# Kernel tuning notes

Hardware: AMD Instinct MI355X
Metric: run time of the kernel (lower is better)

## Reference

```python
import jax, jax.numpy as jnp
import numpy as np
import math

N_EDGES = 3
N_HEADS = 2
ITERS = 2
NEG = -1e9


def setup_inputs() -> dict:
    key = jax.random.key(0)
    ks = jax.random.split(key, 8)
    B, N, D = 4, 2048, 256
    E, H, I = N_EDGES, N_HEADS, ITERS
    s = 1.0 / math.sqrt(D)
    return {
        "nodes_embed": jax.random.normal(ks[0], (B, N, D), jnp.float32),
        "node_adj": jax.random.randint(ks[1], (B, N, N), 0, E + 1, jnp.int32),
        "Wq": jax.random.normal(ks[2], (E, D, D), jnp.float32) * s,
        "bq": jnp.zeros((E, D), jnp.float32),
        "Wk": jax.random.normal(ks[3], (E, D, D), jnp.float32) * s,
        "bk": jnp.zeros((E, D), jnp.float32),
        "gcn_W": jax.random.normal(ks[4], (I, D, D), jnp.float32) * s,
        "gcn_b": jnp.zeros((I, D), jnp.float32),
        "agg_W": jax.random.normal(ks[5], (H * D, D), jnp.float32) * (1.0 / math.sqrt(H * D)),
        "agg_b": jnp.zeros((D,), jnp.float32),
    }


def _forward(nodes_embed, node_adj, Wq, bq, Wk, bk, gcn_W, gcn_b, agg_W, agg_b):
    B, N, D = nodes_embed.shape
    H = N_HEADS
    dk = D // H
    adj = node_adj[:, None]  # [B,1,N,N] broadcast over heads

    # Per-edge-type masked attention accumulation (scores init at 0).
    scores = jnp.zeros((B, H, N, N), nodes_embed.dtype)
    for e in range(N_EDGES):  # small fixed edge-type loop
        q = (nodes_embed @ Wq[e] + bq[e]).reshape(B, N, H, dk).transpose(0, 2, 1, 3)
        k = (nodes_embed @ Wk[e] + bk[e]).reshape(B, N, H, dk).transpose(0, 2, 1, 3)
        raw = jnp.einsum('bhnd,bhmd->bhnm', q, k) / math.sqrt(dk)
        scores = jnp.where(adj == e + 1, scores + raw, scores)

    # Positions never touched (adj==0 or no matching type) stay exactly 0 -> masked.
    scores = jnp.where(scores == 0.0, NEG, scores)
    attn = jax.nn.softmax(scores, axis=-1)  # [B,H,N,N]

    # Per-head GCN stack (parameters shared across heads, as in the torch code).
    outs = []
    for head in range(H):
        a = attn[:, head]  # [B,N,N]
        degs = jnp.sum(a, axis=-1, keepdims=True)  # [B,N,1]
        x = nodes_embed
        for i in range(ITERS):
            h1 = jnp.einsum('bnd,df->bnf', x, gcn_W[i])
            sum_nei = jnp.einsum('bnm,bmf->bnf', a, h1)
            x = x + jax.nn.relu(sum_nei / degs + gcn_b[i])
        outs.append(x)

    out = jnp.concatenate(outs, axis=-1) @ agg_W + agg_b  # [B,N,D]
    graph_attention = jnp.transpose(attn, (1, 0, 2, 3))  # [H,B,N,N]
    return out, graph_attention


def reference(nodes_embed, node_adj, Wq, bq, Wk, bk, gcn_W, gcn_b, agg_W, agg_b):
    return _forward(nodes_embed, node_adj, Wq, bq, Wk, bk, gcn_W, gcn_b, agg_W, agg_b)
```

## Files before the change

### kernel.cpp

```cpp
#include <hip/hip_runtime.h>
#include <stdint.h>
#include <stddef.h>


typedef unsigned short bf16_t;
typedef __attribute__((ext_vector_type(4))) float floatx4;
typedef __attribute__((ext_vector_type(8))) __bf16 bf16x8;
typedef __attribute__((ext_vector_type(4))) unsigned short u16x4;

#define NEGV -1000000000.0f

__device__ __forceinline__ bf16_t f2b(float f) {
  union { float f; uint32_t u; } v; v.f = f;
  uint32_t r = v.u + 0x7FFFu + ((v.u >> 16) & 1u);
  return (bf16_t)(r >> 16);
}

typedef __attribute__((address_space(1))) void gvoid_t;
typedef __attribute__((address_space(3))) void svoid_t;
__device__ __forceinline__ void gll16(const void* g, void* l) {
  __builtin_amdgcn_global_load_lds((gvoid_t*)(g), (svoid_t*)(l), 16, 0, 0);
}

__device__ __forceinline__ bf16x8 lds_frag(const bf16_t* base, int row, int quad) {
  return *(const bf16x8*)(base + (row << 5) + (((quad + (row >> 1)) & 3) << 3));
}

__device__ __forceinline__ void gemm_core(
    const bf16_t* __restrict__ A, int lda, int rowA0,
    const bf16_t* __restrict__ Bt, int ldb, int rowB0,
    int K, bf16_t* lA, bf16_t* lB, floatx4 acc[4][4])
{
  const int lane = threadIdx.x & 63;
  const int wave = threadIdx.x >> 6;
  const int l16  = lane & 15;
  const int quad = lane >> 4;
  const int wm = (wave >> 1) << 6;
  const int wn = (wave & 1) << 6;
  const int srow = (wave << 5) + (lane >> 2);
  const int scol = (((lane & 3) - (srow >> 1)) & 3) << 3;
  const bf16_t* gA0 = A + (size_t)(rowA0 + srow) * lda + scol;
  const bf16_t* gA1 = gA0 + (size_t)16 * lda;
  const bf16_t* gB0 = Bt + (size_t)(rowB0 + srow) * ldb + scol;
  const bf16_t* gB1 = gB0 + (size_t)16 * ldb;
  bf16_t* lA0 = lA + (wave << 5) * 32;
  bf16_t* lA1 = lA0 + 16 * 32;
  bf16_t* lB0 = lB + (wave << 5) * 32;
  bf16_t* lB1 = lB0 + 16 * 32;

  for (int k0 = 0; k0 < K; k0 += 32) {
    __syncthreads();
    gll16(gA0 + k0, lA0);
    gll16(gA1 + k0, lA1);
    gll16(gB0 + k0, lB0);
    gll16(gB1 + k0, lB1);
    __syncthreads();
    bf16x8 af[4], bv[4];
#pragma unroll
    for (int mi = 0; mi < 4; ++mi) af[mi] = lds_frag(lA, wm + mi * 16 + l16, quad);
#pragma unroll
    for (int ni = 0; ni < 4; ++ni) bv[ni] = lds_frag(lB, wn + ni * 16 + l16, quad);
#pragma unroll
    for (int mi = 0; mi < 4; ++mi)
#pragma unroll
      for (int ni = 0; ni < 4; ++ni)
        acc[mi][ni] = __builtin_amdgcn_mfma_f32_16x16x32_bf16(af[mi], bv[ni], acc[mi][ni], 0, 0, 0);
  }
}

__device__ __forceinline__ void gemm_core64(
    const bf16_t* __restrict__ A, int lda, int rowA0,
    const bf16_t* __restrict__ Bt, int ldb, int rowB0,
    int K, bf16_t* lA, bf16_t* lB, floatx4 acc[4][2])
{
  const int lane = threadIdx.x & 63;
  const int wave = threadIdx.x >> 6;
  const int l16  = lane & 15;
  const int quad = lane >> 4;
  const int wn   = wave << 5;
  const int tr   = (wave << 4) + (lane >> 2);
  const int scol = (((lane & 3) - (tr >> 1)) & 3) << 3;
  const bf16_t* gA  = A  + (size_t)(rowA0 + tr) * lda + scol;
  const bf16_t* gB0 = Bt + (size_t)(rowB0 + tr) * ldb + scol;
  const bf16_t* gB1 = gB0 + (size_t)64 * ldb;
  bf16_t* lAd = lA + (wave << 9);
  bf16_t* lB0 = lB + (wave << 9);
  bf16_t* lB1 = lB + 2048 + (wave << 9);

  for (int k0 = 0; k0 < K; k0 += 32) {
    __syncthreads();
    gll16(gA  + k0, lAd);
    gll16(gB0 + k0, lB0);
    gll16(gB1 + k0, lB1);
    __syncthreads();
    bf16x8 af[4], bv[2];
#pragma unroll
    for (int mi = 0; mi < 4; ++mi) af[mi] = lds_frag(lA, mi * 16 + l16, quad);
#pragma unroll
    for (int ni = 0; ni < 2; ++ni) bv[ni] = lds_frag(lB, wn + ni * 16 + l16, quad);
#pragma unroll
    for (int mi = 0; mi < 4; ++mi)
#pragma unroll
      for (int ni = 0; ni < 2; ++ni)
        acc[mi][ni] = __builtin_amdgcn_mfma_f32_16x16x32_bf16(af[mi], bv[ni], acc[mi][ni], 0, 0, 0);
  }
}

#define TILE_IDS \
  const int lane = threadIdx.x & 63; \
  const int wave = threadIdx.x >> 6; \
  const int l16  = lane & 15; \
  const int quad = lane >> 4; \
  const int wm = (wave >> 1) << 6; \
  const int wn = (wave & 1) << 6;

#define TILE_IDS64 \
  const int lane = threadIdx.x & 63; \
  const int wave = threadIdx.x >> 6; \
  const int l16  = lane & 15; \
  const int quad = lane >> 4; \
  const int wn = wave << 5;

#define ZERO44(acc) \
  { const floatx4 z4_ = {0.f, 0.f, 0.f, 0.f}; \
    for (int mi_ = 0; mi_ < 4; ++mi_) for (int ni_ = 0; ni_ < 4; ++ni_) acc[mi_][ni_] = z4_; }
#define ZERO42(acc) \
  { const floatx4 z4_ = {0.f, 0.f, 0.f, 0.f}; \
    for (int mi_ = 0; mi_ < 4; ++mi_) for (int ni_ = 0; ni_ < 2; ++ni_) acc[mi_][ni_] = z4_; }

__global__ __launch_bounds__(256) void k_cast_x(const float* __restrict__ x,
                                                bf16_t* __restrict__ xb) {
  int i = blockIdx.x * 256 + threadIdx.x;
  float4 a = ((const float4*)x)[i * 2];
  float4 b = ((const float4*)x)[i * 2 + 1];
  bf16_t o[8] = { f2b(a.x), f2b(a.y), f2b(a.z), f2b(a.w),
                  f2b(b.x), f2b(b.y), f2b(b.z), f2b(b.w) };
  ((uint4*)xb)[i] = *(uint4*)o;
}

__global__ __launch_bounds__(256) void k_cast_w(
    const float* __restrict__ Wq, const float* __restrict__ Wk,
    const float* __restrict__ gW, const float* __restrict__ aW,
    bf16_t* __restrict__ WqkT, bf16_t* __restrict__ gWT, bf16_t* __restrict__ aWT) {
  int idx = blockIdx.x * 256 + threadIdx.x;
  if (idx < 393216) {
    int zz = idx >> 16, r = idx & 65535;
    int n = r >> 8, k = r & 255;
    const float* src = (zz < 3) ? (Wq + (size_t)zz * 65536) : (Wk + (size_t)(zz - 3) * 65536);
    WqkT[idx] = f2b(src[k * 256 + n]);
  } else if (idx < 524288) {
    int t = idx - 393216;
    int i = t >> 16, r = t & 65535;
    int f = r >> 8, k = r & 255;
    gWT[t] = f2b(gW[(size_t)i * 65536 + k * 256 + f]);
  } else if (idx < 655360) {
    int t = idx - 524288;
    int f = t >> 9, k = t & 511;
    aWT[t] = f2b(aW[k * 256 + f]);
  }
}

__global__ __launch_bounds__(256) void k_gemm_proj(
    const bf16_t* __restrict__ xb, const bf16_t* __restrict__ WqkT,
    const float* __restrict__ bq, const float* __restrict__ bk,
    bf16_t* __restrict__ qcat, bf16_t* __restrict__ kcat) {
  __shared__ bf16_t lA[4096], lB[4096];
  int z = blockIdx.z;
  int e = (z < 3) ? z : z - 3;
  const bf16_t* Wz = WqkT + (size_t)z * 65536;
  const float* bias = ((z < 3) ? bq : bk) + e * 256;
  bf16_t* dst = (z < 3) ? qcat : kcat;
  int bm0 = blockIdx.y * 128, bn0 = blockIdx.x * 128;
  floatx4 acc[4][4];
  ZERO44(acc);
  gemm_core(xb, 256, bm0, Wz, 256, bn0, 256, lA, lB, acc);
  TILE_IDS;
#pragma unroll
  for (int mi = 0; mi < 4; ++mi)
#pragma unroll
    for (int ni = 0; ni < 4; ++ni)
#pragma unroll
      for (int r = 0; r < 4; ++r) {
        int row = bm0 + wm + mi * 16 + quad * 4 + r;
        int col = bn0 + wn + ni * 16 + l16;
        int b = row >> 11, n = row & 2047;
        int h = col >> 7, kk = col & 127;
        float v = acc[mi][ni][r] + bias[col];
        dst[((size_t)((b * 2 + h) * 2048 + n)) * 384 + e * 128 + kk] = f2b(v);
      }
}

__global__ __launch_bounds__(256) void k_scores(
    const bf16_t* __restrict__ qcat, const bf16_t* __restrict__ kcat,
    const int* __restrict__ adj, float* __restrict__ sc) {
  __shared__ bf16_t lA[2048], lB[4096];
  int z = blockIdx.z;
  int h = z >> 2, b = z & 3;
  const bf16_t* A  = qcat + (size_t)(b * 2 + h) * 2048 * 384;
  const bf16_t* Bt = kcat + (size_t)(b * 2 + h) * 2048 * 384;
  const int* adjb = adj + (size_t)b * 2048 * 2048;
  int bm0 = blockIdx.y * 64, bn0 = blockIdx.x * 128;
  TILE_IDS64;

  uint32_t adjv[4][2];
#pragma unroll
  for (int mi = 0; mi < 4; ++mi)
#pragma unroll
    for (int ni = 0; ni < 2; ++ni) {
      int col = bn0 + wn + ni * 16 + l16;
      uint32_t v = 0;
#pragma unroll
      for (int r = 0; r < 4; ++r) {
        int row = bm0 + mi * 16 + quad * 4 + r;
        v |= ((uint32_t)adjb[(size_t)row * 2048 + col] & 3u) << (r * 8);
      }
      adjv[mi][ni] = v;
    }

  floatx4 sel[4][2];
  ZERO42(sel);
  for (int e = 0; e < 3; ++e) {
    floatx4 acc[4][2];
    ZERO42(acc);
    gemm_core64(A + e * 128, 384, bm0, Bt + e * 128, 384, bn0, 128, lA, lB, acc);
#pragma unroll
    for (int mi = 0; mi < 4; ++mi)
#pragma unroll
      for (int ni = 0; ni < 2; ++ni) {
        uint32_t av = adjv[mi][ni];
#pragma unroll
        for (int r = 0; r < 4; ++r) {
          bool m = (((av >> (r * 8)) & 255u) == (uint32_t)(e + 1));
          sel[mi][ni][r] = m ? acc[mi][ni][r] : sel[mi][ni][r];
        }
      }
  }
  const float scale = 0.08838834764831845f;
#pragma unroll
  for (int mi = 0; mi < 4; ++mi)
#pragma unroll
    for (int ni = 0; ni < 2; ++ni)
#pragma unroll
      for (int r = 0; r < 4; ++r) {
        int row = bm0 + mi * 16 + quad * 4 + r;
        int col = bn0 + wn + ni * 16 + l16;
        uint32_t a = (adjv[mi][ni] >> (r * 8)) & 255u;
        float v = (a == 0u) ? NEGV : sel[mi][ni][r] * scale;
        sc[((size_t)z * 2048 + row) * 2048 + col] = v;
      }
}

__global__ __launch_bounds__(256) void k_softmax(float* __restrict__ sc,
                                                 bf16_t* __restrict__ abf) {
  int row = blockIdx.x * 4 + (threadIdx.x >> 6);
  int lane = threadIdx.x & 63;
  float4* p4 = (float4*)(sc + (size_t)row * 2048);
  float4 v[8];
  float mx = -3.4e38f;
#pragma unroll
  for (int j = 0; j < 8; ++j) {
    v[j] = p4[j * 64 + lane];
    mx = fmaxf(mx, fmaxf(fmaxf(v[j].x, v[j].y), fmaxf(v[j].z, v[j].w)));
  }
#pragma unroll
  for (int off = 32; off; off >>= 1) mx = fmaxf(mx, __shfl_xor(mx, off));
  float s = 0.f;
#pragma unroll
  for (int j = 0; j < 8; ++j) {
    v[j].x = __expf(v[j].x - mx); v[j].y = __expf(v[j].y - mx);
    v[j].z = __expf(v[j].z - mx); v[j].w = __expf(v[j].w - mx);
    s += v[j].x + v[j].y + v[j].z + v[j].w;
  }
#pragma unroll
  for (int off = 32; off; off >>= 1) s += __shfl_xor(s, off);
  float inv = 1.0f / s;
  u16x4* b4 = (u16x4*)(abf + (size_t)row * 2048);
#pragma unroll
  for (int j = 0; j < 8; ++j) {
    float4 o;
    o.x = v[j].x * inv; o.y = v[j].y * inv; o.z = v[j].z * inv; o.w = v[j].w * inv;
    p4[j * 64 + lane] = o;
    u16x4 ov = { f2b(o.x), f2b(o.y), f2b(o.z), f2b(o.w) };
    b4[j * 64 + lane] = ov;
  }
}

__global__ __launch_bounds__(256) void k_gemm_bf16T(
    const bf16_t* __restrict__ A, const bf16_t* __restrict__ Wt,
    bf16_t* __restrict__ CT) {
  __shared__ bf16_t lA[4096], lB[4096];
  int bm0 = blockIdx.y * 128, bn0 = blockIdx.x * 128;
  floatx4 acc[4][4];
  ZERO44(acc);
  gemm_core(A, 256, bm0, Wt, 256, bn0, 256, lA, lB, acc);
  TILE_IDS;
#pragma unroll
  for (int mi = 0; mi < 4; ++mi)
#pragma unroll
    for (int ni = 0; ni < 4; ++ni) {
      int row0 = bm0 + wm + mi * 16 + quad * 4;
      int col  = bn0 + wn + ni * 16 + l16;
      int s = row0 >> 11, n = row0 & 2047;
      u16x4 v = { f2b(acc[mi][ni][0]), f2b(acc[mi][ni][1]),
                  f2b(acc[mi][ni][2]), f2b(acc[mi][ni][3]) };
      *(u16x4*)&CT[(size_t)s * 524288 + (size_t)col * 2048 + n] = v;
    }
}

__global__ __launch_bounds__(256) void k_spmm(
    const bf16_t* __restrict__ abf, const bf16_t* __restrict__ h1T,
    long sBb, long sBh, const float* __restrict__ bias,
    const float* __restrict__ rin, long rib, long rih,
    float* __restrict__ rout,
    bf16_t* __restrict__ obf, long obb, long obh, int ldo) {
  __shared__ bf16_t lA[2048], lB[4096];
  int z = blockIdx.z, h = z >> 2, b = z & 3;
  const bf16_t* A  = abf + (size_t)z * 2048 * 2048;
  const bf16_t* Bt = h1T + (size_t)b * sBb + (size_t)h * sBh;
  const float* rz  = rin + (size_t)b * rib + (size_t)h * rih;
  bf16_t* oz = obf + (size_t)b * obb + (size_t)h * obh;
  int bm0 = blockIdx.y * 64, bn0 = blockIdx.x * 128;
  floatx4 acc[4][2];
  ZERO42(acc);
  gemm_core64(A, 2048, bm0, Bt, 2048, bn0, 2048, lA, lB, acc);
  TILE_IDS64;
#pragma unroll
  for (int mi = 0; mi < 4; ++mi)
#pragma unroll
    for (int ni = 0; ni < 2; ++ni)
#pragma unroll
      for (int r = 0; r < 4; ++r) {
        int row = bm0 + mi * 16 + quad * 4 + r;
        int col = bn0 + wn + ni * 16 + l16;
        float s = acc[mi][ni][r] + bias[col];
        float xn = rz[(size_t)row * 256 + col] + fmaxf(s, 0.f);
        if (rout) rout[((size_t)z * 2048 + row) * 256 + col] = xn;
        oz[(size_t)row * ldo + col] = f2b(xn);
      }
}

__global__ __launch_bounds__(256) void k_final(
    const bf16_t* __restrict__ xcat, const bf16_t* __restrict__ aWT,
    const float* __restrict__ ab, float* __restrict__ out) {
  __shared__ bf16_t lA[4096], lB[4096];
  int bm0 = blockIdx.y * 128, bn0 = blockIdx.x * 128;
  floatx4 acc[4][4];
  ZERO44(acc);
  gemm_core(xcat, 512, bm0, aWT, 512, bn0, 512, lA, lB, acc);
  TILE_IDS;
#pragma unroll
  for (int mi = 0; mi < 4; ++mi)
#pragma unroll
    for (int ni = 0; ni < 4; ++ni)
#pragma unroll
      for (int r = 0; r < 4; ++r) {
        int row = bm0 + wm + mi * 16 + quad * 4 + r;
        int col = bn0 + wn + ni * 16 + l16;
        out[(size_t)row * 256 + col] = acc[mi][ni][r] + ab[col];
      }
}

extern "C" void kernel_launch(void* const* d_in, const int* in_sizes, int n_in,
                              void* d_out, int out_size, void* d_ws, size_t ws_size,
                              hipStream_t stream) {
  const float* x   = (const float*)d_in[0];
  const int*   adj = (const int*)d_in[1];
  const float* Wq  = (const float*)d_in[2];
  const float* bq  = (const float*)d_in[3];
  const float* Wk  = (const float*)d_in[4];
  const float* bk  = (const float*)d_in[5];
  const float* gW  = (const float*)d_in[6];
  const float* gb  = (const float*)d_in[7];
  const float* aW  = (const float*)d_in[8];
  const float* ab  = (const float*)d_in[9];
  float* out = (float*)d_out;
  float* sc  = out + 2097152;

  char* w = (char*)d_ws;
  bf16_t* xb   = (bf16_t*)w; w += 4194304;
  bf16_t* WqkT = (bf16_t*)w; w += 786432;
  bf16_t* gWT  = (bf16_t*)w; w += 262144;
  bf16_t* aWT  = (bf16_t*)w; w += 262144;
  bf16_t* qcat = (bf16_t*)w; w += 12582912;
  bf16_t* kcat = (bf16_t*)w; w += 12582912;
  bf16_t* abf  = (bf16_t*)w; w += 67108864;
  bf16_t* h1T  = (bf16_t*)w; w += 4194304;
  float*  x1   = (float*)w;  w += 16777216;
  bf16_t* x1b  = (bf16_t*)w; w += 8388608;
  bf16_t* h1T1 = qcat;
  bf16_t* xcat = kcat;

  k_cast_x<<<1024, 256, 0, stream>>>(x, xb);
  k_cast_w<<<2560, 256, 0, stream>>>(Wq, Wk, gW, aW, WqkT, gWT, aWT);
  k_gemm_proj<<<dim3(2, 64, 6), 256, 0, stream>>>(xb, WqkT, bq, bk, qcat, kcat);
  k_scores<<<dim3(16, 32, 8), 256, 0, stream>>>(qcat, kcat, adj, sc);
  k_softmax<<<4096, 256, 0, stream>>>(sc, abf);
  k_gemm_bf16T<<<dim3(2, 64, 1), 256, 0, stream>>>(xb, gWT, h1T);
  k_spmm<<<dim3(2, 32, 8), 256, 0, stream>>>(abf, h1T, 524288L, 0L, gb,
                                             x, 524288L, 0L, x1,
                                             x1b, 524288L, 2097152L, 256);
  k_gemm_bf16T<<<dim3(2, 128, 1), 256, 0, stream>>>(x1b, gWT + 65536, h1T1);
  k_spmm<<<dim3(2, 32, 8), 256, 0, stream>>>(abf, h1T1, 524288L, 2097152L, gb + 256,
                                             x1, 524288L, 2097152L, nullptr,
                                             xcat, 1048576L, 256L, 512);
  k_final<<<dim3(2, 64, 1), 256, 0, stream>>>(xcat, aWT, ab, out);
}
```

Before: 513.1 us.

## Stage scores as fp16, widen K-tiles with XOR swizzle, remap block grid

k_scores now stages the whole 128-wide K slice per edge type into XOR-swizzled LDS and writes scores as fp16 into the bf16 attention buffer. This halves the score round-trip traffic, since the fp32 write and read of the full score tensor go away. k_softmax reads the fp16 scores, writes fp32 attention to the output, and writes bf16 attention back in place. k_spmm uses 64-wide K steps with swizzled staging, which halves the barrier count, and both kernels use a 1D grid with z fastest so different batches and heads are interleaved. The fp16 score path adds a small precision risk, and masked entries now use -60000 instead of -1e9.

```diff
diff --git a/kernel.cpp b/kernel.cpp
--- a/kernel.cpp
+++ b/kernel.cpp
@@ -8,13 +8,17 @@
 typedef __attribute__((ext_vector_type(8))) __bf16 bf16x8;
 typedef __attribute__((ext_vector_type(4))) unsigned short u16x4;
 
-#define NEGV -1000000000.0f
-
 __device__ __forceinline__ bf16_t f2b(float f) {
   union { float f; uint32_t u; } v; v.f = f;
   uint32_t r = v.u + 0x7FFFu + ((v.u >> 16) & 1u);
   return (bf16_t)(r >> 16);
 }
+__device__ __forceinline__ float h2f(uint16_t u) {
+  union { uint16_t u; _Float16 h; } v; v.u = u; return (float)v.h;
+}
+__device__ __forceinline__ uint16_t f2h(float f) {
+  union { uint16_t u; _Float16 h; } v; v.h = (_Float16)f; return v.u;
+}
 
 typedef __attribute__((address_space(1))) void gvoid_t;
 typedef __attribute__((address_space(3))) void svoid_t;
@@ -22,10 +26,43 @@
   __builtin_amdgcn_global_load_lds((gvoid_t*)(g), (svoid_t*)(l), 16, 0, 0);
 }
 
+
+template <int NR>
+__device__ __forceinline__ void stage128(const bf16_t* G, int ldg, bf16_t* L) {
+  const int lane = threadIdx.x & 63, wave = threadIdx.x >> 6;
+  const int li = lane >> 4, cp = lane & 15;
+#pragma unroll
+  for (int t = 0; t < NR / 16; ++t) {
+    int base_r = wave * (NR / 4) + t * 4;
+    int r = base_r + li;
+    int cl = cp ^ (r & 15);
+    gll16(G + (size_t)r * ldg + cl * 8, L + base_r * 128);
+  }
+}
+template <int NR>
+__device__ __forceinline__ void stage64(const bf16_t* G, int ldg, bf16_t* L) {
+  const int lane = threadIdx.x & 63, wave = threadIdx.x >> 6;
+  const int li = lane >> 3, cp = lane & 7;
+#pragma unroll
+  for (int t = 0; t < NR / 32; ++t) {
+    int base_r = wave * (NR / 4) + t * 8;
+    int r = base_r + li;
+    int cl = cp ^ (r & 7);
+    gll16(G + (size_t)r * ldg + cl * 8, L + base_r * 64);
+  }
+}
+__device__ __forceinline__ bf16x8 frag128(const bf16_t* L, int row, int j, int quad) {
+  int c = ((j << 2) + quad) ^ (row & 15);
+  return *(const bf16x8*)(L + (row << 7) + (c << 3));
+}
+__device__ __forceinline__ bf16x8 frag64(const bf16_t* L, int row, int j, int quad) {
+  int c = ((j << 2) + quad) ^ (row & 7);
+  return *(const bf16x8*)(L + (row << 6) + (c << 3));
+}
+
 __device__ __forceinline__ bf16x8 lds_frag(const bf16_t* base, int row, int quad) {
   return *(const bf16x8*)(base + (row << 5) + (((quad + (row >> 1)) & 3) << 3));
 }
-
 __device__ __forceinline__ void gemm_core(
     const bf16_t* __restrict__ A, int lda, int rowA0,
     const bf16_t* __restrict__ Bt, int ldb, int rowB0,
@@ -68,44 +105,6 @@
   }
 }
 
-__device__ __forceinline__ void gemm_core64(
-    const bf16_t* __restrict__ A, int lda, int rowA0,
-    const bf16_t* __restrict__ Bt, int ldb, int rowB0,
-    int K, bf16_t* lA, bf16_t* lB, floatx4 acc[4][2])
-{
-  const int lane = threadIdx.x & 63;
-  const int wave = threadIdx.x >> 6;
-  const int l16  = lane & 15;
-  const int quad = lane >> 4;
-  const int wn   = wave << 5;
-  const int tr   = (wave << 4) + (lane >> 2);
-  const int scol = (((lane & 3) - (tr >> 1)) & 3) << 3;
-  const bf16_t* gA  = A  + (size_t)(rowA0 + tr) * lda + scol;
-  const bf16_t* gB0 = Bt + (size_t)(rowB0 + tr) * ldb + scol;
-  const bf16_t* gB1 = gB0 + (size_t)64 * ldb;
-  bf16_t* lAd = lA + (wave << 9);
-  bf16_t* lB0 = lB + (wave << 9);
-  bf16_t* lB1 = lB + 2048 + (wave << 9);
-
-  for (int k0 = 0; k0 < K; k0 += 32) {
-    __syncthreads();
-    gll16(gA  + k0, lAd);
-    gll16(gB0 + k0, lB0);
-    gll16(gB1 + k0, lB1);
-    __syncthreads();
-    bf16x8 af[4], bv[2];
-#pragma unroll
-    for (int mi = 0; mi < 4; ++mi) af[mi] = lds_frag(lA, mi * 16 + l16, quad);
-#pragma unroll
-    for (int ni = 0; ni < 2; ++ni) bv[ni] = lds_frag(lB, wn + ni * 16 + l16, quad);
-#pragma unroll
-    for (int mi = 0; mi < 4; ++mi)
-#pragma unroll
-      for (int ni = 0; ni < 2; ++ni)
-        acc[mi][ni] = __builtin_amdgcn_mfma_f32_16x16x32_bf16(af[mi], bv[ni], acc[mi][ni], 0, 0, 0);
-  }
-}
-
 #define TILE_IDS \
   const int lane = threadIdx.x & 63; \
   const int wave = threadIdx.x >> 6; \
@@ -192,14 +191,17 @@
 
 __global__ __launch_bounds__(256) void k_scores(
     const bf16_t* __restrict__ qcat, const bf16_t* __restrict__ kcat,
-    const int* __restrict__ adj, float* __restrict__ sc) {
-  __shared__ bf16_t lA[2048], lB[4096];
-  int z = blockIdx.z;
+    const int* __restrict__ adj, uint16_t* __restrict__ sc16) {
+  __shared__ bf16_t lA[64 * 128];
+  __shared__ bf16_t lB[128 * 128];
+  int i = blockIdx.x;
+  int z = i & 7, t = i >> 3;
+  int y = t & 31, x = t >> 5;
   int h = z >> 2, b = z & 3;
   const bf16_t* A  = qcat + (size_t)(b * 2 + h) * 2048 * 384;
   const bf16_t* Bt = kcat + (size_t)(b * 2 + h) * 2048 * 384;
   const int* adjb = adj + (size_t)b * 2048 * 2048;
-  int bm0 = blockIdx.y * 64, bn0 = blockIdx.x * 128;
+  int bm0 = y * 64, bn0 = x * 128;
   TILE_IDS64;
 
   uint32_t adjv[4][2];
@@ -220,9 +222,25 @@
   floatx4 sel[4][2];
   ZERO42(sel);
   for (int e = 0; e < 3; ++e) {
+    __syncthreads();
+    stage128<64>(A + (size_t)bm0 * 384 + e * 128, 384, lA);
+    stage128<128>(Bt + (size_t)bn0 * 384 + e * 128, 384, lB);
+    __syncthreads();
     floatx4 acc[4][2];
     ZERO42(acc);
-    gemm_core64(A + e * 128, 384, bm0, Bt + e * 128, 384, bn0, 128, lA, lB, acc);
+#pragma unroll
+    for (int j = 0; j < 4; ++j) {
+      bf16x8 af[4], bv[2];
+#pragma unroll
+      for (int mi = 0; mi < 4; ++mi) af[mi] = frag128(lA, mi * 16 + l16, j, quad);
+#pragma unroll
+      for (int ni = 0; ni < 2; ++ni) bv[ni] = frag128(lB, wn + ni * 16 + l16, j, quad);
+#pragma unroll
+      for (int mi = 0; mi < 4; ++mi)
+#pragma unroll
+        for (int ni = 0; ni < 2; ++ni)
+          acc[mi][ni] = __builtin_amdgcn_mfma_f32_16x16x32_bf16(af[mi], bv[ni], acc[mi][ni], 0, 0, 0);
+    }
 #pragma unroll
     for (int mi = 0; mi < 4; ++mi)
 #pragma unroll
@@ -245,43 +263,48 @@
         int row = bm0 + mi * 16 + quad * 4 + r;
         int col = bn0 + wn + ni * 16 + l16;
         uint32_t a = (adjv[mi][ni] >> (r * 8)) & 255u;
-        float v = (a == 0u) ? NEGV : sel[mi][ni][r] * scale;
-        sc[((size_t)z * 2048 + row) * 2048 + col] = v;
-      }
-}
-
-__global__ __launch_bounds__(256) void k_softmax(float* __restrict__ sc,
-                                                 bf16_t* __restrict__ abf) {
+        float v = (a == 0u) ? -60000.0f : sel[mi][ni][r] * scale;
+        sc16[((size_t)z * 2048 + row) * 2048 + col] = f2h(v);
+      }
+}
+
+__global__ __launch_bounds__(256) void k_softmax(uint16_t* sb, float* attn) {
   int row = blockIdx.x * 4 + (threadIdx.x >> 6);
   int lane = threadIdx.x & 63;
-  float4* p4 = (float4*)(sc + (size_t)row * 2048);
-  float4 v[8];
+  uint16_t* p = sb + (size_t)row * 2048;
+  float f[32];
   float mx = -3.4e38f;
 #pragma unroll
-  for (int j = 0; j < 8; ++j) {
-    v[j] = p4[j * 64 + lane];
-    mx = fmaxf(mx, fmaxf(fmaxf(v[j].x, v[j].y), fmaxf(v[j].z, v[j].w)));
+  for (int j = 0; j < 4; ++j) {
+    uint4 hv = ((const uint4*)p)[j * 64 + lane];
+    const uint16_t* hu = (const uint16_t*)&hv;
+#pragma unroll
+    for (int q = 0; q < 8; ++q) {
+      float v = h2f(hu[q]);
+      f[j * 8 + q] = v;
+      mx = fmaxf(mx, v);
+    }
   }
 #pragma unroll
   for (int off = 32; off; off >>= 1) mx = fmaxf(mx, __shfl_xor(mx, off));
   float s = 0.f;
 #pragma unroll
-  for (int j = 0; j < 8; ++j) {
-    v[j].x = __expf(v[j].x - mx); v[j].y = __expf(v[j].y - mx);
-    v[j].z = __expf(v[j].z - mx); v[j].w = __expf(v[j].w - mx);
-    s += v[j].x + v[j].y + v[j].z + v[j].w;
-  }
+  for (int k = 0; k < 32; ++k) { f[k] = __expf(f[k] - mx); s += f[k]; }
 #pragma unroll
   for (int off = 32; off; off >>= 1) s += __shfl_xor(s, off);
   float inv = 1.0f / s;
-  u16x4* b4 = (u16x4*)(abf + (size_t)row * 2048);
-#pragma unroll
-  for (int j = 0; j < 8; ++j) {
-    float4 o;
-    o.x = v[j].x * inv; o.y = v[j].y * inv; o.z = v[j].z * inv; o.w = v[j].w * inv;
-    p4[j * 64 + lane] = o;
-    u16x4 ov = { f2b(o.x), f2b(o.y), f2b(o.z), f2b(o.w) };
-    b4[j * 64 + lane] = ov;
+  float* ar = attn + (size_t)row * 2048;
+#pragma unroll
+  for (int j = 0; j < 4; ++j) {
+    float o[8];
+#pragma unroll
+    for (int q = 0; q < 8; ++q) o[q] = f[j * 8 + q] * inv;
+    ((float4*)ar)[(j * 64 + lane) * 2 + 0] = *(float4*)&o[0];
+    ((float4*)ar)[(j * 64 + lane) * 2 + 1] = *(float4*)&o[4];
+    uint16_t ob[8];
+#pragma unroll
+    for (int q = 0; q < 8; ++q) ob[q] = f2b(o[q]);
+    ((uint4*)p)[j * 64 + lane] = *(uint4*)ob;
   }
 }
 
@@ -313,17 +336,39 @@
     const float* __restrict__ rin, long rib, long rih,
     float* __restrict__ rout,
     bf16_t* __restrict__ obf, long obb, long obh, int ldo) {
-  __shared__ bf16_t lA[2048], lB[4096];
-  int z = blockIdx.z, h = z >> 2, b = z & 3;
+  __shared__ bf16_t lA[64 * 64];
+  __shared__ bf16_t lB[128 * 64];
+  int i = blockIdx.x;
+  int z = i & 7, t = i >> 3;
+  int x = t & 1, y = t >> 1;
+  int h = z >> 2, b = z & 3;
   const bf16_t* A  = abf + (size_t)z * 2048 * 2048;
   const bf16_t* Bt = h1T + (size_t)b * sBb + (size_t)h * sBh;
   const float* rz  = rin + (size_t)b * rib + (size_t)h * rih;
   bf16_t* oz = obf + (size_t)b * obb + (size_t)h * obh;
-  int bm0 = blockIdx.y * 64, bn0 = blockIdx.x * 128;
+  int bm0 = y * 64, bn0 = x * 128;
+  TILE_IDS64;
   floatx4 acc[4][2];
   ZERO42(acc);
-  gemm_core64(A, 2048, bm0, Bt, 2048, bn0, 2048, lA, lB, acc);
-  TILE_IDS64;
+  for (int k0 = 0; k0 < 2048; k0 += 64) {
+    __syncthreads();
+    stage64<64>(A + (size_t)bm0 * 2048 + k0, 2048, lA);
+    stage64<128>(Bt + (size_t)bn0 * 2048 + k0, 2048, lB);
+    __syncthreads();
+#pragma unroll
+    for (int j = 0; j < 2; ++j) {
+      bf16x8 af[4], bv[2];
+#pragma unroll
+      for (int mi = 0; mi < 4; ++mi) af[mi] = frag64(lA, mi * 16 + l16, j, quad);
+#pragma unroll
+      for (int ni = 0; ni < 2; ++ni) bv[ni] = frag64(lB, wn + ni * 16 + l16, j, quad);
+#pragma unroll
+      for (int mi = 0; mi < 4; ++mi)
+#pragma unroll
+        for (int ni = 0; ni < 2; ++ni)
+          acc[mi][ni] = __builtin_amdgcn_mfma_f32_16x16x32_bf16(af[mi], bv[ni], acc[mi][ni], 0, 0, 0);
+    }
+  }
 #pragma unroll
   for (int mi = 0; mi < 4; ++mi)
 #pragma unroll
@@ -393,15 +438,15 @@
   k_cast_x<<<1024, 256, 0, stream>>>(x, xb);
   k_cast_w<<<2560, 256, 0, stream>>>(Wq, Wk, gW, aW, WqkT, gWT, aWT);
   k_gemm_proj<<<dim3(2, 64, 6), 256, 0, stream>>>(xb, WqkT, bq, bk, qcat, kcat);
-  k_scores<<<dim3(16, 32, 8), 256, 0, stream>>>(qcat, kcat, adj, sc);
-  k_softmax<<<4096, 256, 0, stream>>>(sc, abf);
+  k_scores<<<4096, 256, 0, stream>>>(qcat, kcat, adj, (uint16_t*)abf);
+  k_softmax<<<4096, 256, 0, stream>>>((uint16_t*)abf, sc);
   k_gemm_bf16T<<<dim3(2, 64, 1), 256, 0, stream>>>(xb, gWT, h1T);
-  k_spmm<<<dim3(2, 32, 8), 256, 0, stream>>>(abf, h1T, 524288L, 0L, gb,
-                                             x, 524288L, 0L, x1,
-                                             x1b, 524288L, 2097152L, 256);
+  k_spmm<<<512, 256, 0, stream>>>(abf, h1T, 524288L, 0L, gb,
+                                  x, 524288L, 0L, x1,
+                                  x1b, 524288L, 2097152L, 256);
   k_gemm_bf16T<<<dim3(2, 128, 1), 256, 0, stream>>>(x1b, gWT + 65536, h1T1);
-  k_spmm<<<dim3(2, 32, 8), 256, 0, stream>>>(abf, h1T1, 524288L, 2097152L, gb + 256,
-                                             x1, 524288L, 2097152L, nullptr,
-                                             xcat, 1048576L, 256L, 512);
+  k_spmm<<<512, 256, 0, stream>>>(abf, h1T1, 524288L, 2097152L, gb + 256,
+                                  x1, 524288L, 2097152L, nullptr,
+                                  xcat, 1048576L, 256L, 512);
   k_final<<<dim3(2, 64, 1), 256, 0, stream>>>(xcat, aWT, ab, out);
 }
```

Result: faster. 415.9 us (-18.9%).
